# Kernel tuning notes

Measured on AMD Instinct MI355X. Metric: run time of the kernel, lower is better.

## Reference

```python
import jax, jax.numpy as jnp
import numpy as np

TEMPERATURE = 0.5
EPS = 1e-12  # torch F.normalize eps


def _l2_normalize(x, eps=EPS):
    n = jnp.linalg.norm(x, axis=1, keepdims=True)
    return x / jnp.maximum(n, eps)


def setup_inputs() -> dict:
    key = jax.random.key(0)
    k1, k2 = jax.random.split(key)
    B, D = 4096, 512
    return {
        "polyline_embs": jax.random.normal(k1, (B, D), dtype=jnp.float32),
        "c_embs": jax.random.normal(k2, (B, D), dtype=jnp.float32),
    }


def reference(polyline_embs, c_embs):
    b = polyline_embs.shape[0]
    # double-normalization in the original (F.normalize then cosine_similarity)
    # is idempotent on unit vectors, so sim = Z @ Z^T with Z unit-normalized.
    z = _l2_normalize(jnp.concatenate([polyline_embs, c_embs], axis=0))  # [2B, D]
    sim = z @ z.T  # [2B, 2B] cosine similarity
    # positives: diag offsets +B and -B
    idx = jnp.arange(b)
    sim_ij = sim[idx, idx + b]
    sim_ji = sim[idx + b, idx]
    positives = jnp.concatenate([sim_ij, sim_ji], axis=0)  # [2B]
    nominator = jnp.exp(positives / TEMPERATURE)
    mask = 1.0 - jnp.eye(2 * b, dtype=sim.dtype)
    denominator = jnp.sum(mask * jnp.exp(sim / TEMPERATURE), axis=1)  # [2B]
    all_losses = -jnp.log(nominator / denominator)
    return jnp.sum(all_losses) / (2 * b)
```

## Files before the change

### kernel.cpp

```cpp
#include <hip/hip_runtime.h>
#include <hip/hip_bf16.h>

#define B_ROWS 4096
#define D_DIM  512
#define N_ROWS 8192
#define BM 128
#define BN 128
#define BKB 128
#define NBLK (N_ROWS / BM)
#define NPAIR (NBLK * (NBLK + 1) / 2)

typedef float f32x4 __attribute__((ext_vector_type(4)));

__global__ __launch_bounds__(256) void prep_kernel(
    const float* __restrict__ poly, const float* __restrict__ cemb,
    unsigned char* __restrict__ Z, float* __restrict__ row_sum,
    float* __restrict__ pos, unsigned int* __restrict__ counter)
{
    const int r = blockIdx.x;
    const int t = threadIdx.x;
    const float* prow = poly + (size_t)r * D_DIM;
    const float* crow = cemb + (size_t)r * D_DIM;

    const float2 pv = *(const float2*)(prow + 2 * t);
    const float2 cv = *(const float2*)(crow + 2 * t);

    float ssp = pv.x * pv.x + pv.y * pv.y;
    float ssc = cv.x * cv.x + cv.y * cv.y;
    float dt  = pv.x * cv.x + pv.y * cv.y;

    #pragma unroll
    for (int m = 1; m < 64; m <<= 1) {
        ssp += __shfl_xor(ssp, m);
        ssc += __shfl_xor(ssc, m);
        dt  += __shfl_xor(dt,  m);
    }
    __shared__ float red[3][4];
    const int wave = t >> 6;
    if ((t & 63) == 0) { red[0][wave] = ssp; red[1][wave] = ssc; red[2][wave] = dt; }
    __syncthreads();
    ssp = red[0][0] + red[0][1] + red[0][2] + red[0][3];
    ssc = red[1][0] + red[1][1] + red[1][2] + red[1][3];
    dt  = red[2][0] + red[2][1] + red[2][2] + red[2][3];

    const float sp = 1.0f / fmaxf(sqrtf(ssp), 1e-12f);
    const float sc = 1.0f / fmaxf(sqrtf(ssc), 1e-12f);

    unsigned char* zp = Z + (size_t)r * D_DIM;
    unsigned char* zc = Z + (size_t)(r + B_ROWS) * D_DIM;
    const int pk = __builtin_amdgcn_cvt_pk_fp8_f32(pv.x * sp, pv.y * sp, 0, false);
    const int ck = __builtin_amdgcn_cvt_pk_fp8_f32(cv.x * sc, cv.y * sc, 0, false);
    *(unsigned short*)(zp + 2 * t) = (unsigned short)(pk & 0xffff);
    *(unsigned short*)(zc + 2 * t) = (unsigned short)(ck & 0xffff);

    if (t == 0) {
        pos[r] = dt * sp * sc;
        row_sum[2 * r]     = 0.0f;
        row_sum[2 * r + 1] = 0.0f;
        if (r == 0) *counter = 0u;
    }
}

__global__ __launch_bounds__(256) void sim_kernel(
    const unsigned char* __restrict__ Z, float* __restrict__ row_sum,
    const float* __restrict__ pos, float* __restrict__ out,
    unsigned int* __restrict__ counter)
{
    __shared__ __align__(16) unsigned char As[BM * BKB];
    __shared__ __align__(16) unsigned char Bs[BN * BKB];
    __shared__ float rAcc[BM];
    __shared__ float cAcc[BN];
    __shared__ unsigned int lastFlag;

    const int t0 = blockIdx.x;
    int bi = (int)((129.0f - sqrtf(16641.0f - 8.0f * (float)t0)) * 0.5f);
    #define CFN(b) ((b) * (129 - (b)) / 2)
    while (CFN(bi + 1) <= t0) ++bi;
    while (CFN(bi) > t0) --bi;
    const int bj = bi + (t0 - CFN(bi));
    #undef CFN
    const bool diag = (bi == bj);

    const int ibase = bi * BM;
    const int jbase = bj * BN;
    const int tid   = threadIdx.x;

    const int srow = tid >> 3;
    const int gchk = (tid & 7) ^ (srow & 7);

    const int wave = tid >> 6;
    const int lane = tid & 63;
    const int wi = (wave >> 1) * 64;
    const int wj = (wave & 1) * 64;
    const int quad = lane >> 4;
    const int c    = lane & 15;

    f32x4 acc[4][4] = {};

    for (int k0 = 0; k0 < D_DIM; k0 += BKB) {
        #pragma unroll
        for (int it = 0; it < 4; ++it) {
            const int row = it * 32 + srow;
            const unsigned char* ga = Z + (size_t)(ibase + row) * D_DIM + k0 + gchk * 16;
            __builtin_amdgcn_global_load_lds(
                (const __attribute__((address_space(1))) void*)ga,
                (__attribute__((address_space(3))) void*)(As + it * 4096 + tid * 16),
                16, 0, 0);
        }
        if (!diag) {
            #pragma unroll
            for (int it = 0; it < 4; ++it) {
                const int row = it * 32 + srow;
                const unsigned char* gb = Z + (size_t)(jbase + row) * D_DIM + k0 + gchk * 16;
                __builtin_amdgcn_global_load_lds(
                    (const __attribute__((address_space(1))) void*)gb,
                    (__attribute__((address_space(3))) void*)(Bs + it * 4096 + tid * 16),
                    16, 0, 0);
            }
        }
        __syncthreads();

        const unsigned char* bsrc = diag ? As : Bs;
        #pragma unroll
        for (int kk = 0; kk < BKB; kk += 32) {
            const int sw  = ((kk >> 4) + (quad >> 1)) ^ (c & 7);
            const int sub = (quad & 1) * 8;
            long a[4], b[4];
            #pragma unroll
            for (int ti = 0; ti < 4; ++ti)
                a[ti] = *(const long*)&As[(wi + ti * 16 + c) * BKB + sw * 16 + sub];
            #pragma unroll
            for (int tj = 0; tj < 4; ++tj)
                b[tj] = *(const long*)&bsrc[(wj + tj * 16 + c) * BKB + sw * 16 + sub];
            #pragma unroll
            for (int ti = 0; ti < 4; ++ti)
                #pragma unroll
                for (int tj = 0; tj < 4; ++tj)
                    acc[ti][tj] = __builtin_amdgcn_mfma_f32_16x16x32_fp8_fp8(
                        a[ti], b[tj], acc[ti][tj], 0, 0, 0);
        }
        __syncthreads();
    }

    if (tid < BM) { rAcc[tid] = 0.0f; cAcc[tid] = 0.0f; }
    __syncthreads();

    const float K2 = 2.885390081777927f;
    float col[4] = {0.0f, 0.0f, 0.0f, 0.0f};
    #pragma unroll
    for (int ti = 0; ti < 4; ++ti) {
        const int li = wi + ti * 16 + quad * 4;
        #pragma unroll
        for (int r = 0; r < 4; ++r) {
            const int gi = ibase + li + r;
            float v = 0.0f;
            #pragma unroll
            for (int tj = 0; tj < 4; ++tj) {
                const int gj = jbase + wj + tj * 16 + c;
                const float e = (gj > gi) ? exp2f(K2 * acc[ti][tj][r]) : 0.0f;
                v += e;
                col[tj] += e;
            }
            v += __shfl_xor(v, 1);
            v += __shfl_xor(v, 2);
            v += __shfl_xor(v, 4);
            v += __shfl_xor(v, 8);
            if (c == 0)
                atomicAdd(&rAcc[li + r], v);
        }
    }
    #pragma unroll
    for (int tj = 0; tj < 4; ++tj) {
        float w = col[tj];
        w += __shfl_xor(w, 16);
        w += __shfl_xor(w, 32);
        if (quad == 0)
            atomicAdd(&cAcc[wj + tj * 16 + c], w);
    }
    __syncthreads();

    if (tid < BM)
        atomicAdd(&row_sum[ibase + tid], rAcc[tid]);
    else
        atomicAdd(&row_sum[jbase + tid - BM], cAcc[tid - BM]);

    __syncthreads();
    if (tid == 0) {
        unsigned int old = __hip_atomic_fetch_add(
            counter, 1u, __ATOMIC_RELAXED, __HIP_MEMORY_SCOPE_AGENT);
        lastFlag = (old == NPAIR - 1) ? 1u : 0u;
    }
    __syncthreads();
    if (lastFlag) {
        float accL = 0.0f, accP = 0.0f;
        for (int i = tid; i < N_ROWS; i += 256) {
            const float rs = __hip_atomic_load(
                &row_sum[i], __ATOMIC_RELAXED, __HIP_MEMORY_SCOPE_AGENT);
            accL += __logf(rs);
        }
        for (int r = tid; r < B_ROWS; r += 256)
            accP += pos[r];
        #pragma unroll
        for (int m = 1; m < 64; m <<= 1) {
            accL += __shfl_xor(accL, m);
            accP += __shfl_xor(accP, m);
        }
        if (lane == 0) { rAcc[wave] = accL; cAcc[wave] = accP; }
        __syncthreads();
        if (tid == 0) {
            float L = 0.0f, P = 0.0f;
            #pragma unroll
            for (int w = 0; w < 4; ++w) { L += rAcc[w]; P += cAcc[w]; }
            out[0] = (L - 4.0f * P) / (float)N_ROWS;
        }
    }
}

extern "C" void kernel_launch(void* const* d_in, const int* in_sizes, int n_in,
                              void* d_out, int out_size, void* d_ws, size_t ws_size,
                              hipStream_t stream) {
    const float* poly = (const float*)d_in[0];
    const float* cemb = (const float*)d_in[1];

    unsigned char* Z       = (unsigned char*)d_ws;
    float*         row_sum = (float*)((char*)d_ws + (size_t)N_ROWS * D_DIM);
    float*         pos     = row_sum + N_ROWS;
    unsigned int*  counter = (unsigned int*)(pos + B_ROWS);
    float*         out     = (float*)d_out;

    prep_kernel<<<B_ROWS, 256, 0, stream>>>(poly, cemb, Z, row_sum, pos, counter);
    sim_kernel<<<NPAIR, 256, 0, stream>>>(Z, row_sum, pos, out, counter);
}
```

Measured before the change: 131.6 us.

## Double-buffer LDS tiles with smaller K step to overlap loads and MFMA

Halves the K tile to 64 bytes and allocates two LDS buffers so the next K slice is loaded via global_load_lds while the current slice is multiplied. The swizzle pattern is reworked for the 64-byte row stride. The goal is to hide global-load latency behind MFMA work in place of a serial load-sync-compute loop. LDS use stays at 32KB, but the loop runs twice as many iterations and barriers, and the new swizzle could introduce bank conflicts.

After: 135.3 us. 2.9% more time.

```diff
diff --git a/kernel.cpp b/kernel.cpp
--- a/kernel.cpp
+++ b/kernel.cpp
@@ -6,7 +6,8 @@
 #define N_ROWS 8192
 #define BM 128
 #define BN 128
-#define BKB 128
+#define BKB 64
+#define NK  (D_DIM / BKB)
 #define NBLK (N_ROWS / BM)
 #define NPAIR (NBLK * (NBLK + 1) / 2)
 
@@ -66,8 +67,8 @@
     const float* __restrict__ pos, float* __restrict__ out,
     unsigned int* __restrict__ counter)
 {
-    __shared__ __align__(16) unsigned char As[BM * BKB];
-    __shared__ __align__(16) unsigned char Bs[BN * BKB];
+    __shared__ __align__(16) unsigned char As[2][BM * BKB];
+    __shared__ __align__(16) unsigned char Bs[2][BN * BKB];
     __shared__ float rAcc[BM];
     __shared__ float cAcc[BN];
     __shared__ unsigned int lastFlag;
@@ -85,8 +86,8 @@
     const int jbase = bj * BN;
     const int tid   = threadIdx.x;
 
-    const int srow = tid >> 3;
-    const int gchk = (tid & 7) ^ (srow & 7);
+    const int srow4 = tid >> 2;
+    const int sg    = (tid & 3) ^ ((srow4 >> 1) & 3);
 
     const int wave = tid >> 6;
     const int lane = tid & 63;
@@ -94,44 +95,47 @@
     const int wj = (wave & 1) * 64;
     const int quad = lane >> 4;
     const int c    = lane & 15;
+    const int fkey = (c >> 1) & 3;
 
     f32x4 acc[4][4] = {};
 
-    for (int k0 = 0; k0 < D_DIM; k0 += BKB) {
-        #pragma unroll
-        for (int it = 0; it < 4; ++it) {
-            const int row = it * 32 + srow;
-            const unsigned char* ga = Z + (size_t)(ibase + row) * D_DIM + k0 + gchk * 16;
+    auto stage = [&](int buf, int k0) {
+        #pragma unroll
+        for (int it = 0; it < 2; ++it) {
+            const int row = it * 64 + srow4;
+            const unsigned char* ga = Z + (size_t)(ibase + row) * D_DIM + k0 + sg * 16;
             __builtin_amdgcn_global_load_lds(
                 (const __attribute__((address_space(1))) void*)ga,
-                (__attribute__((address_space(3))) void*)(As + it * 4096 + tid * 16),
+                (__attribute__((address_space(3))) void*)(&As[buf][0] + it * 4096 + tid * 16),
                 16, 0, 0);
         }
         if (!diag) {
             #pragma unroll
-            for (int it = 0; it < 4; ++it) {
-                const int row = it * 32 + srow;
-                const unsigned char* gb = Z + (size_t)(jbase + row) * D_DIM + k0 + gchk * 16;
+            for (int it = 0; it < 2; ++it) {
+                const int row = it * 64 + srow4;
+                const unsigned char* gb = Z + (size_t)(jbase + row) * D_DIM + k0 + sg * 16;
                 __builtin_amdgcn_global_load_lds(
                     (const __attribute__((address_space(1))) void*)gb,
-                    (__attribute__((address_space(3))) void*)(Bs + it * 4096 + tid * 16),
+                    (__attribute__((address_space(3))) void*)(&Bs[buf][0] + it * 4096 + tid * 16),
                     16, 0, 0);
             }
         }
-        __syncthreads();
-
-        const unsigned char* bsrc = diag ? As : Bs;
-        #pragma unroll
-        for (int kk = 0; kk < BKB; kk += 32) {
-            const int sw  = ((kk >> 4) + (quad >> 1)) ^ (c & 7);
-            const int sub = (quad & 1) * 8;
+    };
+
+    auto compute = [&](int buf) {
+        const unsigned char* abase = &As[buf][0];
+        const unsigned char* bbase = diag ? &As[buf][0] : &Bs[buf][0];
+        #pragma unroll
+        for (int kk = 0; kk < 2; ++kk) {
+            const int sl  = ((quad >> 1) + 2 * kk) ^ fkey;
+            const int off = sl * 16 + (quad & 1) * 8;
             long a[4], b[4];
             #pragma unroll
             for (int ti = 0; ti < 4; ++ti)
-                a[ti] = *(const long*)&As[(wi + ti * 16 + c) * BKB + sw * 16 + sub];
+                a[ti] = *(const long*)&abase[(wi + ti * 16 + c) * BKB + off];
             #pragma unroll
             for (int tj = 0; tj < 4; ++tj)
-                b[tj] = *(const long*)&bsrc[(wj + tj * 16 + c) * BKB + sw * 16 + sub];
+                b[tj] = *(const long*)&bbase[(wj + tj * 16 + c) * BKB + off];
             #pragma unroll
             for (int ti = 0; ti < 4; ++ti)
                 #pragma unroll
@@ -139,6 +143,16 @@
                     acc[ti][tj] = __builtin_amdgcn_mfma_f32_16x16x32_fp8_fp8(
                         a[ti], b[tj], acc[ti][tj], 0, 0, 0);
         }
+    };
+
+    stage(0, 0);
+    __syncthreads();
+    #pragma unroll
+    for (int i = 0; i < NK; ++i) {
+        const int cur = i & 1;
+        if (i < NK - 1)
+            stage(cur ^ 1, (i + 1) * BKB);
+        compute(cur);
         __syncthreads();
     }
 
```
